# Kernel tuning notes

Measured on AMD Instinct MI355X. Metric: run time of the kernel, lower is better.

The kernel has to match this reference:

```python
import jax, jax.numpy as jnp
import numpy as np

N = 100000      # nodes
E = 1600000     # edges (avg degree 16)
D_IN, D_H1, D_H2, D_OUT = 512, 256, 256, 64


def setup_inputs() -> dict:
    key = jax.random.key(0)
    ks = jax.random.split(key, 8)
    x = jax.random.normal(ks[0], (N, D_IN), dtype=jnp.float32)
    row = jax.random.randint(ks[1], (E,), 0, N, dtype=jnp.int32)
    col = jax.random.randint(ks[2], (E,), 0, N, dtype=jnp.int32)
    vals = jax.random.uniform(ks[3], (E,), dtype=jnp.float32)
    # xavier-normal-ish scaling for weights
    W1 = jax.random.normal(ks[4], (D_IN, D_H1), dtype=jnp.float32) * np.sqrt(2.0 / (D_IN + D_H1))
    W2 = jax.random.normal(ks[5], (D_H1, D_H2), dtype=jnp.float32) * np.sqrt(2.0 / (D_H1 + D_H2))
    W3 = jax.random.normal(ks[6], (D_H2, D_OUT), dtype=jnp.float32) * np.sqrt(2.0 / (D_H2 + D_OUT))
    b1 = jnp.zeros((D_H1,), dtype=jnp.float32)
    b2 = jnp.zeros((D_H2,), dtype=jnp.float32)
    b3 = jnp.zeros((D_OUT,), dtype=jnp.float32)
    return {"x": x, "row": row, "col": col, "vals": vals,
            "W1": W1, "b1": b1, "W2": W2, "b2": b2, "W3": W3, "b3": b3}


def reference(x, row, col, vals, W1, b1, W2, b2, W3, b3):
    n = x.shape[0]

    def spmm(h):
        # out[i] = sum_{e: row[e]==i} vals[e] * h[col[e]]  (COO spmm)
        return jax.ops.segment_sum(vals[:, None] * h[col], row, num_segments=n)

    # layer 1: linear -> spmm -> relu  (dropout p=0 -> identity)
    h = jax.nn.relu(spmm(x @ W1 + b1))
    # layer 2
    h = jax.nn.relu(spmm(h @ W2 + b2))
    # output layer: no activation, no dropout
    return spmm(h @ W3 + b3)
```

## Files before the change

### kernel.cpp

```cpp
#include <hip/hip_runtime.h>

typedef _Float16 f16;
typedef _Float16 f16x4 __attribute__((ext_vector_type(4)));
typedef _Float16 f16x8 __attribute__((ext_vector_type(8)));
typedef float f32x4 __attribute__((ext_vector_type(4)));

#define DEVI __device__ __forceinline__

static constexpr int CAP = 64;

DEVI f16x8 cvt8(float4 a, float4 b) {
  f16x8 r;
  r[0] = (f16)a.x; r[1] = (f16)a.y; r[2] = (f16)a.z; r[3] = (f16)a.w;
  r[4] = (f16)b.x; r[5] = (f16)b.y; r[6] = (f16)b.z; r[7] = (f16)b.w;
  return r;
}

__global__ __launch_bounds__(256)
void prep_w(const float* __restrict__ W1, const float* __restrict__ W2,
            const float* __restrict__ W3, f16* __restrict__ WT1,
            f16* __restrict__ WT2, f16* __restrict__ WT3) {
  int t = blockIdx.x * 256 + threadIdx.x;
  if (t < 131072) {
    int n = t >> 9, k = t & 511;
    WT1[t] = (f16)W1[k * 256 + n];
  } else if (t < 131072 + 65536) {
    int u = t - 131072; int n = u >> 8, k = u & 255;
    WT2[u] = (f16)W2[k * 256 + n];
  } else if (t < 131072 + 65536 + 16384) {
    int u = t - 131072 - 65536; int n = u >> 8, k = u & 255;
    WT3[u] = (f16)W3[k * 64 + n];
  }
}

__global__ __launch_bounds__(256)
void build_slots(const int* __restrict__ row, const int* __restrict__ col,
                 const float* __restrict__ vals, int* __restrict__ cnt,
                 int2* __restrict__ slots, int E) {
  int e = blockIdx.x * 256 + threadIdx.x;
  if (e >= E) return;
  int r = row[e];
  int p = atomicAdd(&cnt[r], 1);
  if (p < CAP) slots[(size_t)r * CAP + p] = make_int2(col[e], __float_as_int(vals[e]));
}

template <int NT, int WN, int KI, bool AF32>
__global__ __launch_bounds__(256, 3)
void gemm_direct(const void* __restrict__ Ap, const f16* __restrict__ WT,
                 const float* __restrict__ bias, f16* __restrict__ C,
                 int M, int N) {
  constexpr int K = KI * 32;
  const int tid = threadIdx.x;
  const int wave = tid >> 6, lane = tid & 63;
  const int quad = lane >> 4, l16 = lane & 15;
  const int wn = (WN == 1) ? 0 : (wave & 1);
  const int wm = (WN == 1) ? wave : (wave >> 1);
  constexpr int RPB = (4 / WN) * 32;
  const int r0 = blockIdx.x * RPB + wm * 32;
  const int n0 = wn * (NT * 16);

  f32x4 acc[2][NT];
#pragma unroll
  for (int mt = 0; mt < 2; ++mt)
#pragma unroll
    for (int nt = 0; nt < NT; ++nt) {
      f32x4 z = {0.f, 0.f, 0.f, 0.f};
      acc[mt][nt] = z;
    }

  const int ar0 = min(r0 + l16, M - 1);
  const int ar1 = min(r0 + 16 + l16, M - 1);

#pragma unroll 2
  for (int kb = 0; kb < KI; ++kb) {
    const int k0 = kb * 32 + quad * 8;
    f16x8 af[2];
    if constexpr (AF32) {
      const float* Af = (const float*)Ap;
      const float4* p0 = (const float4*)(Af + (size_t)ar0 * K + k0);
      const float4* p1 = (const float4*)(Af + (size_t)ar1 * K + k0);
      float4 u0 = p0[0], u1 = p0[1];
      float4 v0 = p1[0], v1 = p1[1];
      af[0] = cvt8(u0, u1);
      af[1] = cvt8(v0, v1);
    } else {
      const f16* Ah = (const f16*)Ap;
      af[0] = *(const f16x8*)(Ah + (size_t)ar0 * K + k0);
      af[1] = *(const f16x8*)(Ah + (size_t)ar1 * K + k0);
    }
    f16x8 bf[NT];
#pragma unroll
    for (int nt = 0; nt < NT; ++nt)
      bf[nt] = *(const f16x8*)(WT + (size_t)(n0 + nt * 16 + l16) * K + k0);
#pragma unroll
    for (int mt = 0; mt < 2; ++mt)
#pragma unroll
      for (int nt = 0; nt < NT; ++nt)
        acc[mt][nt] = __builtin_amdgcn_mfma_f32_16x16x32_f16(af[mt], bf[nt], acc[mt][nt], 0, 0, 0);
  }

  float bv[NT];
#pragma unroll
  for (int nt = 0; nt < NT; ++nt)
    bv[nt] = bias[n0 + nt * 16 + l16];
#pragma unroll
  for (int mt = 0; mt < 2; ++mt) {
#pragma unroll
    for (int nt = 0; nt < NT; ++nt) {
      const int colg = n0 + nt * 16 + l16;
#pragma unroll
      for (int r = 0; r < 4; ++r) {
        int grow = r0 + mt * 16 + quad * 4 + r;
        if (grow < M)
          C[(size_t)grow * N + colg] = (f16)(acc[mt][nt][r] + bv[nt]);
      }
    }
  }
}

__global__ __launch_bounds__(256)
void spmm_relu256(const f16* __restrict__ T, const int2* __restrict__ slots,
                  const int* __restrict__ cnt, f16* __restrict__ H, int nrows) {
  const int wave = threadIdx.x >> 6, lane = threadIdx.x & 63;
  const int i = blockIdx.x * 4 + wave;
  if (i >= nrows) return;
  const int c = min(cnt[i], CAP);
  const int2* sl = slots + (size_t)i * CAP;
  const int half = lane >> 5, fl = lane & 31;

  float a[8];
#pragma unroll
  for (int k = 0; k < 8; ++k) a[k] = 0.f;

  int j = 0;
  for (; j + 8 <= c; j += 8) {
    int2 e0 = sl[j + half], e1 = sl[j + 2 + half];
    int2 e2 = sl[j + 4 + half], e3 = sl[j + 6 + half];
    f16x8 u0 = *(const f16x8*)(T + (size_t)e0.x * 256 + fl * 8);
    f16x8 u1 = *(const f16x8*)(T + (size_t)e1.x * 256 + fl * 8);
    f16x8 u2 = *(const f16x8*)(T + (size_t)e2.x * 256 + fl * 8);
    f16x8 u3 = *(const f16x8*)(T + (size_t)e3.x * 256 + fl * 8);
    float v0 = __int_as_float(e0.y), v1 = __int_as_float(e1.y);
    float v2 = __int_as_float(e2.y), v3 = __int_as_float(e3.y);
#pragma unroll
    for (int k = 0; k < 8; ++k)
      a[k] += v0 * (float)u0[k] + v1 * (float)u1[k] + v2 * (float)u2[k] + v3 * (float)u3[k];
  }
  for (; j < c; j += 2) {
    int jj = j + half;
    int2 e = sl[min(jj, c - 1)];
    float v = (jj < c) ? __int_as_float(e.y) : 0.f;
    f16x8 u = *(const f16x8*)(T + (size_t)e.x * 256 + fl * 8);
#pragma unroll
    for (int k = 0; k < 8; ++k) a[k] += v * (float)u[k];
  }
#pragma unroll
  for (int k = 0; k < 8; ++k) a[k] += __shfl_xor(a[k], 32, 64);
  if (half == 0) {
    f16x8 o;
#pragma unroll
    for (int k = 0; k < 8; ++k) o[k] = (f16)fmaxf(a[k], 0.f);
    *(f16x8*)(H + (size_t)i * 256 + fl * 8) = o;
  }
}

__global__ __launch_bounds__(256)
void spmm_out64(const f16* __restrict__ T, const int2* __restrict__ slots,
                const int* __restrict__ cnt, float* __restrict__ out, int nrows) {
  const int wave = threadIdx.x >> 6, lane = threadIdx.x & 63;
  const int i = blockIdx.x * 4 + wave;
  if (i >= nrows) return;
  const int c = min(cnt[i], CAP);
  const int2* sl = slots + (size_t)i * CAP;
  const int sub = lane >> 4, fl = lane & 15;

  float a[4];
#pragma unroll
  for (int k = 0; k < 4; ++k) a[k] = 0.f;

  int j = 0;
  for (; j + 8 <= c; j += 8) {
    int2 e0 = sl[j + sub], e1 = sl[j + 4 + sub];
    f16x4 u0 = *(const f16x4*)(T + (size_t)e0.x * 64 + fl * 4);
    f16x4 u1 = *(const f16x4*)(T + (size_t)e1.x * 64 + fl * 4);
    float v0 = __int_as_float(e0.y), v1 = __int_as_float(e1.y);
#pragma unroll
    for (int k = 0; k < 4; ++k) a[k] += v0 * (float)u0[k] + v1 * (float)u1[k];
  }
  for (; j < c; j += 4) {
    int jj = j + sub;
    int2 e = sl[min(jj, c - 1)];
    float v = (jj < c) ? __int_as_float(e.y) : 0.f;
    f16x4 u = *(const f16x4*)(T + (size_t)e.x * 64 + fl * 4);
#pragma unroll
    for (int k = 0; k < 4; ++k) a[k] += v * (float)u[k];
  }
#pragma unroll
  for (int k = 0; k < 4; ++k) {
    a[k] += __shfl_xor(a[k], 16, 64);
    a[k] += __shfl_xor(a[k], 32, 64);
  }
  if (sub == 0) {
    float4 o = make_float4(a[0], a[1], a[2], a[3]);
    *(float4*)(out + (size_t)i * 64 + fl * 4) = o;
  }
}

extern "C" void kernel_launch(void* const* d_in, const int* in_sizes, int n_in,
                              void* d_out, int out_size, void* d_ws, size_t ws_size,
                              hipStream_t stream) {
  const float* x    = (const float*)d_in[0];
  const int*   row  = (const int*)d_in[1];
  const int*   col  = (const int*)d_in[2];
  const float* vals = (const float*)d_in[3];
  const float* W1   = (const float*)d_in[4];
  const float* b1   = (const float*)d_in[5];
  const float* W2   = (const float*)d_in[6];
  const float* b2   = (const float*)d_in[7];
  const float* W3   = (const float*)d_in[8];
  const float* b3   = (const float*)d_in[9];
  float* out = (float*)d_out;

  const int N = in_sizes[0] / 512;
  const int E = in_sizes[1];

  char* ws = (char*)d_ws;
  const size_t MiB = 1ull << 20;
  int*  cnt   = (int*)ws;
  int2* slots = (int2*)(ws + 1 * MiB);
  f16*  WT1   = (f16*)(ws + 52 * MiB);
  f16*  WT2   = WT1 + 256 * 512;
  f16*  WT3   = WT2 + 256 * 256;
  f16*  T     = (f16*)(ws + 53 * MiB);
  f16*  H     = (f16*)(ws + 104 * MiB);

  hipMemsetAsync(cnt, 0, (size_t)N * sizeof(int), stream);
  prep_w<<<(131072 + 65536 + 16384 + 255) / 256, 256, 0, stream>>>(W1, W2, W3, WT1, WT2, WT3);
  build_slots<<<(E + 255) / 256, 256, 0, stream>>>(row, col, vals, cnt, slots, E);

  const int g12 = (N + 63) / 64;
  const int g3  = (N + 127) / 128;
  const int gs  = (N + 3) / 4;

  gemm_direct<8, 2, 16, true><<<g12, 256, 0, stream>>>(x, WT1, b1, T, N, 256);
  spmm_relu256<<<gs, 256, 0, stream>>>(T, slots, cnt, H, N);
  gemm_direct<8, 2, 8, false><<<g12, 256, 0, stream>>>(H, WT2, b2, T, N, 256);
  spmm_relu256<<<gs, 256, 0, stream>>>(T, slots, cnt, H, N);
  gemm_direct<4, 1, 8, false><<<g3, 256, 0, stream>>>(H, WT3, b3, T, N, 64);
  spmm_out64<<<gs, 256, 0, stream>>>(T, slots, cnt, out, N);
}
```

Baseline: 907.8 us.

## Stage GEMM tiles through LDS via direct global-to-LDS loads; deepen SpMM gathers

```diff
diff --git a/kernel.cpp b/kernel.cpp
--- a/kernel.cpp
+++ b/kernel.cpp
@@ -8,6 +8,12 @@
 #define DEVI __device__ __forceinline__
 
 static constexpr int CAP = 64;
+
+DEVI void g2l16(const void* g, void* l) {
+  __builtin_amdgcn_global_load_lds(
+      (const __attribute__((address_space(1))) void*)g,
+      (__attribute__((address_space(3))) void*)l, 16, 0, 0);
+}
 
 DEVI f16x8 cvt8(float4 a, float4 b) {
   f16x8 r;
@@ -45,19 +51,22 @@
 }
 
 template <int NT, int WN, int KI, bool AF32>
-__global__ __launch_bounds__(256, 3)
-void gemm_direct(const void* __restrict__ Ap, const f16* __restrict__ WT,
-                 const float* __restrict__ bias, f16* __restrict__ C,
-                 int M, int N) {
+__global__ __launch_bounds__(256)
+void gemm_lds(const void* __restrict__ Ap, const f16* __restrict__ WT,
+              const float* __restrict__ bias, f16* __restrict__ C,
+              int M, int N) {
   constexpr int K = KI * 32;
+  constexpr int RPB = (4 / WN) * 32;
+  constexpr int BN = WN * NT * 16;
+  __shared__ alignas(16) char AsB[RPB * 32 * (AF32 ? 4 : 2)];
+  __shared__ alignas(16) char BsB[BN * 32 * 2];
+
   const int tid = threadIdx.x;
   const int wave = tid >> 6, lane = tid & 63;
   const int quad = lane >> 4, l16 = lane & 15;
   const int wn = (WN == 1) ? 0 : (wave & 1);
   const int wm = (WN == 1) ? wave : (wave >> 1);
-  constexpr int RPB = (4 / WN) * 32;
-  const int r0 = blockIdx.x * RPB + wm * 32;
-  const int n0 = wn * (NT * 16);
+  const int r0 = blockIdx.x * RPB;
 
   f32x4 acc[2][NT];
 #pragma unroll
@@ -68,49 +77,73 @@
       acc[mt][nt] = z;
     }
 
-  const int ar0 = min(r0 + l16, M - 1);
-  const int ar1 = min(r0 + 16 + l16, M - 1);
-
-#pragma unroll 2
   for (int kb = 0; kb < KI; ++kb) {
-    const int k0 = kb * 32 + quad * 8;
-    f16x8 af[2];
     if constexpr (AF32) {
       const float* Af = (const float*)Ap;
-      const float4* p0 = (const float4*)(Af + (size_t)ar0 * K + k0);
-      const float4* p1 = (const float4*)(Af + (size_t)ar1 * K + k0);
-      float4 u0 = p0[0], u1 = p0[1];
-      float4 v0 = p1[0], v1 = p1[1];
-      af[0] = cvt8(u0, u1);
-      af[1] = cvt8(v0, v1);
+      const int rowg = min(r0 + wave * 16 + l16, M - 1);
+#pragma unroll
+      for (int t = 0; t < 2; ++t) {
+        const float* gp = Af + (size_t)rowg * K + kb * 32 + (t * 4 + quad) * 4;
+        g2l16(gp, AsB + wave * 2048 + t * 1024);
+      }
     } else {
       const f16* Ah = (const f16*)Ap;
-      af[0] = *(const f16x8*)(Ah + (size_t)ar0 * K + k0);
-      af[1] = *(const f16x8*)(Ah + (size_t)ar1 * K + k0);
+#pragma unroll
+      for (int t = 0; t < RPB / 64; ++t) {
+        const int blk = wave * (RPB / 64) + t;
+        const int rowg = min(r0 + blk * 16 + l16, M - 1);
+        const f16* gp = Ah + (size_t)rowg * K + kb * 32 + quad * 8;
+        g2l16(gp, AsB + blk * 1024);
+      }
+    }
+#pragma unroll
+    for (int t = 0; t < BN / 64; ++t) {
+      const int blk = wave * (BN / 64) + t;
+      const int n = blk * 16 + l16;
+      const f16* gp = WT + (size_t)n * K + kb * 32 + quad * 8;
+      g2l16(gp, BsB + blk * 1024);
+    }
+    __syncthreads();
+
+    f16x8 af[2];
+#pragma unroll
+    for (int mt = 0; mt < 2; ++mt) {
+      const int blk = wm * 2 + mt;
+      if constexpr (AF32) {
+        const float4* p = (const float4*)(AsB + blk * 2048);
+        float4 a0 = p[quad * 32 + l16];
+        float4 a1 = p[quad * 32 + 16 + l16];
+        af[mt] = cvt8(a0, a1);
+      } else {
+        af[mt] = *(const f16x8*)(AsB + blk * 1024 + (quad * 16 + l16) * 16);
+      }
     }
     f16x8 bf[NT];
 #pragma unroll
-    for (int nt = 0; nt < NT; ++nt)
-      bf[nt] = *(const f16x8*)(WT + (size_t)(n0 + nt * 16 + l16) * K + k0);
+    for (int nt = 0; nt < NT; ++nt) {
+      const int blk = wn * NT + nt;
+      bf[nt] = *(const f16x8*)(BsB + blk * 1024 + (quad * 16 + l16) * 16);
+    }
 #pragma unroll
     for (int mt = 0; mt < 2; ++mt)
 #pragma unroll
       for (int nt = 0; nt < NT; ++nt)
         acc[mt][nt] = __builtin_amdgcn_mfma_f32_16x16x32_f16(af[mt], bf[nt], acc[mt][nt], 0, 0, 0);
+    __syncthreads();
   }
 
   float bv[NT];
 #pragma unroll
   for (int nt = 0; nt < NT; ++nt)
-    bv[nt] = bias[n0 + nt * 16 + l16];
+    bv[nt] = bias[wn * NT * 16 + nt * 16 + l16];
 #pragma unroll
   for (int mt = 0; mt < 2; ++mt) {
 #pragma unroll
     for (int nt = 0; nt < NT; ++nt) {
-      const int colg = n0 + nt * 16 + l16;
+      const int colg = wn * NT * 16 + nt * 16 + l16;
 #pragma unroll
       for (int r = 0; r < 4; ++r) {
-        int grow = r0 + mt * 16 + quad * 4 + r;
+        const int grow = r0 + wm * 32 + mt * 16 + quad * 4 + r;
         if (grow < M)
           C[(size_t)grow * N + colg] = (f16)(acc[mt][nt][r] + bv[nt]);
       }
@@ -133,6 +166,21 @@
   for (int k = 0; k < 8; ++k) a[k] = 0.f;
 
   int j = 0;
+  for (; j + 16 <= c; j += 16) {
+    int2 e[8];
+#pragma unroll
+    for (int t = 0; t < 8; ++t) e[t] = sl[j + 2 * t + half];
+    f16x8 u[8];
+#pragma unroll
+    for (int t = 0; t < 8; ++t)
+      u[t] = *(const f16x8*)(T + (size_t)e[t].x * 256 + fl * 8);
+#pragma unroll
+    for (int t = 0; t < 8; ++t) {
+      const float v = __int_as_float(e[t].y);
+#pragma unroll
+      for (int k = 0; k < 8; ++k) a[k] += v * (float)u[t][k];
+    }
+  }
   for (; j + 8 <= c; j += 8) {
     int2 e0 = sl[j + half], e1 = sl[j + 2 + half];
     int2 e2 = sl[j + 4 + half], e3 = sl[j + 6 + half];
@@ -147,9 +195,9 @@
       a[k] += v0 * (float)u0[k] + v1 * (float)u1[k] + v2 * (float)u2[k] + v3 * (float)u3[k];
   }
   for (; j < c; j += 2) {
-    int jj = j + half;
+    const int jj = j + half;
     int2 e = sl[min(jj, c - 1)];
-    float v = (jj < c) ? __int_as_float(e.y) : 0.f;
+    const float v = (jj < c) ? __int_as_float(e.y) : 0.f;
     f16x8 u = *(const f16x8*)(T + (size_t)e.x * 256 + fl * 8);
 #pragma unroll
     for (int k = 0; k < 8; ++k) a[k] += v * (float)u[k];
@@ -179,18 +227,25 @@
   for (int k = 0; k < 4; ++k) a[k] = 0.f;
 
   int j = 0;
-  for (; j + 8 <= c; j += 8) {
-    int2 e0 = sl[j + sub], e1 = sl[j + 4 + sub];
-    f16x4 u0 = *(const f16x4*)(T + (size_t)e0.x * 64 + fl * 4);
-    f16x4 u1 = *(const f16x4*)(T + (size_t)e1.x * 64 + fl * 4);
-    float v0 = __int_as_float(e0.y), v1 = __int_as_float(e1.y);
-#pragma unroll
-    for (int k = 0; k < 4; ++k) a[k] += v0 * (float)u0[k] + v1 * (float)u1[k];
+  for (; j + 16 <= c; j += 16) {
+    int2 e[4];
+#pragma unroll
+    for (int t = 0; t < 4; ++t) e[t] = sl[j + 4 * t + sub];
+    f16x4 u[4];
+#pragma unroll
+    for (int t = 0; t < 4; ++t)
+      u[t] = *(const f16x4*)(T + (size_t)e[t].x * 64 + fl * 4);
+#pragma unroll
+    for (int t = 0; t < 4; ++t) {
+      const float v = __int_as_float(e[t].y);
+#pragma unroll
+      for (int k = 0; k < 4; ++k) a[k] += v * (float)u[t][k];
+    }
   }
   for (; j < c; j += 4) {
-    int jj = j + sub;
+    const int jj = j + sub;
     int2 e = sl[min(jj, c - 1)];
-    float v = (jj < c) ? __int_as_float(e.y) : 0.f;
+    const float v = (jj < c) ? __int_as_float(e.y) : 0.f;
     f16x4 u = *(const f16x4*)(T + (size_t)e.x * 64 + fl * 4);
 #pragma unroll
     for (int k = 0; k < 4; ++k) a[k] += v * (float)u[k];
@@ -242,10 +297,10 @@
   const int g3  = (N + 127) / 128;
   const int gs  = (N + 3) / 4;
 
-  gemm_direct<8, 2, 16, true><<<g12, 256, 0, stream>>>(x, WT1, b1, T, N, 256);
+  gemm_lds<8, 2, 16, true><<<g12, 256, 0, stream>>>(x, WT1, b1, T, N, 256);
   spmm_relu256<<<gs, 256, 0, stream>>>(T, slots, cnt, H, N);
-  gemm_direct<8, 2, 8, false><<<g12, 256, 0, stream>>>(H, WT2, b2, T, N, 256);
+  gemm_lds<8, 2, 8, false><<<g12, 256, 0, stream>>>(H, WT2, b2, T, N, 256);
   spmm_relu256<<<gs, 256, 0, stream>>>(T, slots, cnt, H, N);
-  gemm_direct<4, 1, 8, false><<<g3, 256, 0, stream>>>(H, WT3, b3, T, N, 64);
+  gemm_lds<4, 1, 8, false><<<g3, 256, 0, stream>>>(H, WT3, b3, T, N, 64);
   spmm_out64<<<gs, 256, 0, stream>>>(T, slots, cnt, out, N);
 }
```

Result: faster. 831.8 us (-8.4%).
